# Kernel optimization log

Measured on AMD Instinct MI355X. Metric: run time of the kernel, lower is better.

Reference implementation:

```python
import jax, jax.numpy as jnp
import numpy as np

B, N, F, H, OUT = 64, 512, 128, 256, 6


def setup_inputs() -> dict:
    key = jax.random.key(0)
    ks = jax.random.split(key, 20)
    s = 0.02
    inp = {
        "x": jax.random.normal(ks[0], (B * N, F), dtype=jnp.float32),
        "edge_index": jax.random.randint(ks[1], (2, 16), 0, B * N),
        "edge_weight": jax.random.uniform(ks[2], (16,), dtype=jnp.float32),
        "batch": jnp.repeat(jnp.arange(B, dtype=jnp.int64), N),
        "sigma": jax.random.uniform(ks[3], (1,), dtype=jnp.float32),
        "Wg": s * jax.random.normal(ks[4], (F, F)), "bg": jnp.zeros((F,)),
        "Wrel0": s * jax.random.normal(ks[5], (F, H)), "Wroot0": s * jax.random.normal(ks[6], (F, H)), "brel0": jnp.zeros((H,)),
        "Wrel1": s * jax.random.normal(ks[7], (H, H)), "Wroot1": s * jax.random.normal(ks[8], (H, H)), "brel1": jnp.zeros((H,)),
        "Wrel2": s * jax.random.normal(ks[9], (H, H)), "Wroot2": s * jax.random.normal(ks[10], (H, H)), "brel2": jnp.zeros((H,)),
        "W1": s * jax.random.normal(ks[11], (H, H)), "b1": jnp.zeros((H,)),
        "Wout": s * jax.random.normal(ks[12], (H, OUT)), "bout": jnp.zeros((OUT,)),
    }
    return inp


def _forward(x, sigma, Wg, bg, Wrel0, Wroot0, brel0, Wrel1, Wroot1, brel1,
             Wrel2, Wroot2, brel2, W1, b1, Wout, bout):
    # gdmLinear
    h = x @ Wg + bg                      # [B*N, F]
    hw = h.reshape(B, N, -1)             # to_dense_batch (equal-size windows)
    # pairwise squared distances per window -> Gaussian kernel
    sq = jnp.sum(hw * hw, axis=-1)       # [B, N]
    dist = jnp.maximum(sq[:, :, None] + sq[:, None, :]
                       - 2.0 * jnp.einsum('bnf,bmf->bnm', hw, hw), 0.0)
    A = jnp.exp(-dist / (2.0 * sigma[0] ** 2))   # [B, N, N], all > 0
    A = A * (1.0 - jnp.eye(N, dtype=A.dtype))    # nonzero extraction drops self-loops

    def conv(h, Wrel, Wroot, brel):
        # GraphConv: out_i = W_rel @ sum_j A[j,i] * h_j + b_rel + W_root @ h_i
        agg = jnp.einsum('bji,bjf->bif', A, h)
        return agg @ Wrel + brel + h @ Wroot

    h = hw
    h = jax.nn.relu(conv(h, Wrel0, Wroot0, brel0))
    h = jax.nn.relu(conv(h, Wrel1, Wroot1, brel1))
    h = conv(h, Wrel2, Wroot2, brel2)
    g = jnp.mean(h, axis=1)              # global_mean_pool (equal-size graphs)
    g = jax.nn.relu(g @ W1 + b1)
    return g @ Wout + bout               # [B, OUT]


def reference(x, edge_index, edge_weight, batch, sigma, Wg, bg,
              Wrel0, Wroot0, brel0, Wrel1, Wroot1, brel1,
              Wrel2, Wroot2, brel2, W1, b1, Wout, bout):
    # edge_index / edge_weight / batch inputs are recomputed internally by GdmGNN
    return _forward(x, sigma, Wg, bg, Wrel0, Wroot0, brel0, Wrel1, Wroot1, brel1,
                    Wrel2, Wroot2, brel2, W1, b1, Wout, bout)
```

## Files before the change

### kernel.cpp

```cpp
#include <hip/hip_runtime.h>
#include <math.h>

#define Bsz 64
#define Nn 512
#define Ff 128
#define Hh 256
#define OUTD 6
#define MTOT (Bsz * Nn)

typedef __bf16 bf16x8 __attribute__((ext_vector_type(8)));
typedef float f32x4 __attribute__((ext_vector_type(4)));
typedef int int4v __attribute__((ext_vector_type(4)));
typedef unsigned short ushort4v __attribute__((ext_vector_type(4)));

__device__ __forceinline__ unsigned short f2bf(float f) {
    unsigned u = __float_as_uint(f);
    u += 0x7FFFu + ((u >> 16) & 1u);
    return (unsigned short)(u >> 16);
}
__device__ __forceinline__ float bf2f(unsigned short s) {
    return __uint_as_float(((unsigned)s) << 16);
}

#define SWZ(r) (((r) ^ ((r) >> 2)) & 3)

__device__ __forceinline__ void async_ld16(const unsigned short* g, unsigned short* l) {
    __builtin_amdgcn_global_load_lds(
        (const __attribute__((address_space(1))) void*)g,
        (__attribute__((address_space(3))) void*)l,
        16, 0, 0);
}

#define LDH 40
#define TSZ (128 * 32)
#define AGP 136
#define AGP1 264

__global__ __launch_bounds__(512) void fused_l0(
    const unsigned short* __restrict__ h0T,
    const unsigned short* __restrict__ Arows,
    const unsigned short* __restrict__ h0b,
    const unsigned short* __restrict__ WrelT0,
    const unsigned short* __restrict__ WrootT0,
    const float* __restrict__ brel0,
    unsigned short* __restrict__ h1b,
    unsigned short* __restrict__ h1T)
{
    int id = blockIdx.x;
    int b = id & 63;
    int nt = id >> 6;
    int n0g = nt * 128;
    long nodeBase = (long)b * Nn + n0g;

    const unsigned short* HT = h0T + (long)b * Ff * Nn;
    const unsigned short* AR = Arows + (long)b * Nn * Nn;

    __shared__ unsigned short SA[2 * TSZ];
    __shared__ unsigned short SB[2 * TSZ];
    __shared__ unsigned short aggL[128 * AGP];

    int tid = threadIdx.x;
    int lane = tid & 63;
    int wave = tid >> 6;
    int quad = lane >> 4, l16 = lane & 15;
    int wm = (wave >> 1) * 32, wn = (wave & 1) * 64;
    int sr = lane >> 2, sc = lane & 3;

    {
        f32x4 acc[2][4] = {};
        auto issue = [&](int g) {
            int kk = g << 5;
            unsigned short* Ad = SA + (g & 1) * TSZ;
            unsigned short* Bd = SB + (g & 1) * TSZ;
            int r = wave * 16 + sr;
            int c = sc ^ SWZ(r);
            async_ld16(HT + (long)r * Nn + kk + c * 8, Ad + (wave * 16) * 32);
            async_ld16(AR + (long)(n0g + r) * Nn + kk + c * 8, Bd + (wave * 16) * 32);
        };
        issue(0);
        for (int g = 0; g < (Nn >> 5); ++g) {
            __syncthreads();
            if (g + 1 < (Nn >> 5)) issue(g + 1);
            const unsigned short* Ab = SA + (g & 1) * TSZ;
            const unsigned short* Bb = SB + (g & 1) * TSZ;
            bf16x8 af[2], bfr[4];
            #pragma unroll
            for (int i = 0; i < 2; ++i) {
                int r = wm + i * 16 + l16;
                af[i] = *(const bf16x8*)&Ab[r * 32 + (quad ^ SWZ(r)) * 8];
            }
            #pragma unroll
            for (int j = 0; j < 4; ++j) {
                int r = wn + j * 16 + l16;
                bfr[j] = *(const bf16x8*)&Bb[r * 32 + (quad ^ SWZ(r)) * 8];
            }
            #pragma unroll
            for (int i = 0; i < 2; ++i)
                #pragma unroll
                for (int j = 0; j < 4; ++j)
                    acc[i][j] = __builtin_amdgcn_mfma_f32_16x16x32_bf16(
                        af[i], bfr[j], acc[i][j], 0, 0, 0);
        }
        #pragma unroll
        for (int i = 0; i < 2; ++i) {
            int f = wm + i * 16 + quad * 4;
            #pragma unroll
            for (int j = 0; j < 4; ++j) {
                int nl = wn + j * 16 + l16;
                f32x4 v = acc[i][j];
                ushort4v p;
                p[0] = f2bf(v[0]); p[1] = f2bf(v[1]);
                p[2] = f2bf(v[2]); p[3] = f2bf(v[3]);
                *(ushort4v*)&aggL[nl * AGP + f] = p;
            }
        }
    }
    __syncthreads();

    for (int half = 0; half < 2; ++half) {
        int m0 = half * 128;
        f32x4 acc[2][4] = {};
        auto issue = [&](int g) {
            unsigned short* Ad = SA + (g & 1) * TSZ;
            int r = wave * 16 + sr;
            int c = sc ^ SWZ(r);
            if (g < 4) {
                async_ld16(WrelT0 + (long)(m0 + r) * Ff + (g << 5) + c * 8,
                           Ad + (wave * 16) * 32);
            } else {
                async_ld16(WrootT0 + (long)(m0 + r) * Ff + ((g - 4) << 5) + c * 8,
                           Ad + (wave * 16) * 32);
                unsigned short* Bd = SB + (g & 1) * TSZ;
                async_ld16(h0b + (nodeBase + r) * Ff + ((g - 4) << 5) + c * 8,
                           Bd + (wave * 16) * 32);
            }
        };
        issue(0);
        for (int g = 0; g < 8; ++g) {
            __syncthreads();
            if (g + 1 < 8) issue(g + 1);
            const unsigned short* Ab = SA + (g & 1) * TSZ;
            bf16x8 af[2], bfr[4];
            #pragma unroll
            for (int i = 0; i < 2; ++i) {
                int r = wm + i * 16 + l16;
                af[i] = *(const bf16x8*)&Ab[r * 32 + (quad ^ SWZ(r)) * 8];
            }
            if (g < 4) {
                #pragma unroll
                for (int j = 0; j < 4; ++j) {
                    int nl = wn + j * 16 + l16;
                    bfr[j] = *(const bf16x8*)&aggL[nl * AGP + (g << 5) + quad * 8];
                }
            } else {
                const unsigned short* Bb = SB + (g & 1) * TSZ;
                #pragma unroll
                for (int j = 0; j < 4; ++j) {
                    int r = wn + j * 16 + l16;
                    bfr[j] = *(const bf16x8*)&Bb[r * 32 + (quad ^ SWZ(r)) * 8];
                }
            }
            #pragma unroll
            for (int i = 0; i < 2; ++i)
                #pragma unroll
                for (int j = 0; j < 4; ++j)
                    acc[i][j] = __builtin_amdgcn_mfma_f32_16x16x32_bf16(
                        af[i], bfr[j], acc[i][j], 0, 0, 0);
        }
        #pragma unroll
        for (int i = 0; i < 2; ++i) {
            int of = m0 + wm + i * 16 + quad * 4;
            float b0 = brel0[of + 0], b1 = brel0[of + 1];
            float b2 = brel0[of + 2], b3 = brel0[of + 3];
            #pragma unroll
            for (int j = 0; j < 4; ++j) {
                int nl = wn + j * 16 + l16;
                f32x4 v = acc[i][j];
                float o0 = fmaxf(v[0] + b0, 0.f), o1 = fmaxf(v[1] + b1, 0.f);
                float o2 = fmaxf(v[2] + b2, 0.f), o3 = fmaxf(v[3] + b3, 0.f);
                ushort4v p;
                p[0] = f2bf(o0); p[1] = f2bf(o1); p[2] = f2bf(o2); p[3] = f2bf(o3);
                *(ushort4v*)&h1b[(nodeBase + nl) * Hh + of] = p;
                long base = ((long)b * Hh) * 512 + n0g + nl;
                h1T[base + (long)(of + 0) * 512] = p[0];
                h1T[base + (long)(of + 1) * 512] = p[1];
                h1T[base + (long)(of + 2) * 512] = p[2];
                h1T[base + (long)(of + 3) * 512] = p[3];
            }
        }
    }
}

__global__ __launch_bounds__(512) void fused_l1(
    const unsigned short* __restrict__ h1T,
    const unsigned short* __restrict__ Arows,
    const unsigned short* __restrict__ h1b,
    const unsigned short* __restrict__ WrelT1,
    const unsigned short* __restrict__ WrootT1,
    const float* __restrict__ brel1,
    const float* __restrict__ w,
    float* __restrict__ vpart, float* __restrict__ mpart)
{
    constexpr int ATS = 256 * 32;
    constexpr int BTS = 64 * 32;

    int id = blockIdx.x;
    int b = id & 63;
    int nt = id >> 6;
    int n0g = nt * 64;
    long nodeBase = (long)b * Nn + n0g;

    const unsigned short* HT = h1T + (long)b * Hh * Nn;
    const unsigned short* AR = Arows + (long)b * Nn * Nn;

    __shared__ unsigned short SA[2 * ATS];
    __shared__ unsigned short SB[2 * BTS];
    __shared__ unsigned short aggL[64 * AGP1];

    int tid = threadIdx.x;
    int lane = tid & 63;
    int wave = tid >> 6;
    int quad = lane >> 4, l16 = lane & 15;
    int wm = wave * 32;
    int sr = lane >> 2, sc = lane & 3;

    {
        f32x4 acc[2][4] = {};
        auto issue = [&](int g) {
            int kk = g << 5;
            unsigned short* Ad = SA + (g & 1) * ATS;
            int r = wave * 16 + sr;
            int c = sc ^ SWZ(r);
            async_ld16(HT + (long)r * Nn + kk + c * 8, Ad + (wave * 16) * 32);
            int r2 = 128 + r;
            int c2 = sc ^ SWZ(r2);
            async_ld16(HT + (long)r2 * Nn + kk + c2 * 8, Ad + (128 + wave * 16) * 32);
            if (wave < 4) {
                unsigned short* Bd = SB + (g & 1) * BTS;
                async_ld16(AR + (long)(n0g + r) * Nn + kk + c * 8,
                           Bd + (wave * 16) * 32);
            }
        };
        issue(0);
        for (int g = 0; g < 16; ++g) {
            __syncthreads();
            if (g + 1 < 16) issue(g + 1);
            const unsigned short* Ab = SA + (g & 1) * ATS;
            const unsigned short* Bb = SB + (g & 1) * BTS;
            bf16x8 af[2], bfr[4];
            #pragma unroll
            for (int i = 0; i < 2; ++i) {
                int r = wm + i * 16 + l16;
                af[i] = *(const bf16x8*)&Ab[r * 32 + (quad ^ SWZ(r)) * 8];
            }
            #pragma unroll
            for (int j = 0; j < 4; ++j) {
                int r = j * 16 + l16;
                bfr[j] = *(const bf16x8*)&Bb[r * 32 + (quad ^ SWZ(r)) * 8];
            }
            #pragma unroll
            for (int i = 0; i < 2; ++i)
                #pragma unroll
                for (int j = 0; j < 4; ++j)
                    acc[i][j] = __builtin_amdgcn_mfma_f32_16x16x32_bf16(
                        af[i], bfr[j], acc[i][j], 0, 0, 0);
        }
        #pragma unroll
        for (int i = 0; i < 2; ++i) {
            int f = wm + i * 16 + quad * 4;
            #pragma unroll
            for (int j = 0; j < 4; ++j) {
                int nl = j * 16 + l16;
                f32x4 v = acc[i][j];
                ushort4v p;
                p[0] = f2bf(v[0]); p[1] = f2bf(v[1]);
                p[2] = f2bf(v[2]); p[3] = f2bf(v[3]);
                *(ushort4v*)&aggL[nl * AGP1 + f] = p;
            }
        }
    }
    __syncthreads();

    f32x4 acc[2][4] = {};
    auto issue2 = [&](int g) {
        const unsigned short* Wp = (g < 8) ? WrelT1 : WrootT1;
        int kk = (g & 7) << 5;
        unsigned short* Ad = SA + (g & 1) * ATS;
        int r = wave * 16 + sr;
        int c = sc ^ SWZ(r);
        async_ld16(Wp + (long)r * Hh + kk + c * 8, Ad + (wave * 16) * 32);
        int r2 = 128 + r;
        int c2 = sc ^ SWZ(r2);
        async_ld16(Wp + (long)r2 * Hh + kk + c2 * 8, Ad + (128 + wave * 16) * 32);
        if (g >= 8 && wave < 4) {
            unsigned short* Bd = SB + (g & 1) * BTS;
            async_ld16(h1b + (nodeBase + r) * Hh + kk + c * 8, Bd + (wave * 16) * 32);
        }
    };
    issue2(0);
    for (int g = 0; g < 16; ++g) {
        __syncthreads();
        if (g + 1 < 16) issue2(g + 1);
        const unsigned short* Ab = SA + (g & 1) * ATS;
        bf16x8 af[2], bfr[4];
        #pragma unroll
        for (int i = 0; i < 2; ++i) {
            int r = wm + i * 16 + l16;
            af[i] = *(const bf16x8*)&Ab[r * 32 + (quad ^ SWZ(r)) * 8];
        }
        if (g < 8) {
            #pragma unroll
            for (int j = 0; j < 4; ++j) {
                int nl = j * 16 + l16;
                bfr[j] = *(const bf16x8*)&aggL[nl * AGP1 + (g << 5) + quad * 8];
            }
        } else {
            const unsigned short* Bb = SB + (g & 1) * BTS;
            #pragma unroll
            for (int j = 0; j < 4; ++j) {
                int r = j * 16 + l16;
                bfr[j] = *(const bf16x8*)&Bb[r * 32 + (quad ^ SWZ(r)) * 8];
            }
        }
        #pragma unroll
        for (int i = 0; i < 2; ++i)
            #pragma unroll
            for (int j = 0; j < 4; ++j)
                acc[i][j] = __builtin_amdgcn_mfma_f32_16x16x32_bf16(
                    af[i], bfr[j], acc[i][j], 0, 0, 0);
    }

    #pragma unroll
    for (int i = 0; i < 2; ++i) {
        int lf = wm + i * 16 + quad * 4;
        float b0 = brel1[lf + 0], b1 = brel1[lf + 1];
        float b2 = brel1[lf + 2], b3 = brel1[lf + 3];
        float vp0 = 0.f, vp1 = 0.f, vp2 = 0.f, vp3 = 0.f;
        float mp0 = 0.f, mp1 = 0.f, mp2 = 0.f, mp3 = 0.f;
        #pragma unroll
        for (int j = 0; j < 4; ++j) {
            long node = nodeBase + j * 16 + l16;
            f32x4 v = acc[i][j];
            float o0 = fmaxf(v[0] + b0, 0.f), o1 = fmaxf(v[1] + b1, 0.f);
            float o2 = fmaxf(v[2] + b2, 0.f), o3 = fmaxf(v[3] + b3, 0.f);
            float h0v = bf2f(f2bf(o0)), h1v = bf2f(f2bf(o1));
            float h2v = bf2f(f2bf(o2)), h3v = bf2f(f2bf(o3));
            float wv = w[node];
            vp0 += wv * h0v; vp1 += wv * h1v; vp2 += wv * h2v; vp3 += wv * h3v;
            mp0 += h0v; mp1 += h1v; mp2 += h2v; mp3 += h3v;
        }
        #pragma unroll
        for (int m = 1; m < 16; m <<= 1) {
            vp0 += __shfl_xor(vp0, m); vp1 += __shfl_xor(vp1, m);
            vp2 += __shfl_xor(vp2, m); vp3 += __shfl_xor(vp3, m);
            mp0 += __shfl_xor(mp0, m); mp1 += __shfl_xor(mp1, m);
            mp2 += __shfl_xor(mp2, m); mp3 += __shfl_xor(mp3, m);
        }
        if (l16 == 0) {
            long o = ((long)(b * 8 + nt)) * Hh + lf;
            float4 vv = {vp0, vp1, vp2, vp3};
            float4 mm = {mp0, mp1, mp2, mp3};
            *(float4*)&vpart[o] = vv;
            *(float4*)&mpart[o] = mm;
        }
    }
}

__global__ __launch_bounds__(256) void prep_h0(
    const float* __restrict__ x, const float* __restrict__ Wg,
    const float* __restrict__ bg,
    const float* __restrict__ Wrel0, const float* __restrict__ Wroot0,
    const float* __restrict__ Wrel1, const float* __restrict__ Wroot1,
    unsigned short* __restrict__ T0, unsigned short* __restrict__ T1,
    unsigned short* __restrict__ T2, unsigned short* __restrict__ T3,
    float* __restrict__ w,
    unsigned short* __restrict__ h0b, unsigned short* __restrict__ h0T,
    float* __restrict__ sqv)
{
    if (blockIdx.x < 896) {
        int idx = blockIdx.x * 256 + threadIdx.x;
        if (idx >= 196608) { w[idx - 196608] = 0.f; return; }
        const float* src; unsigned short* dst; int kin; int e;
        if      (idx <  32768) { src = Wrel0;  dst = T0; kin = 128; e = idx; }
        else if (idx <  65536) { src = Wroot0; dst = T1; kin = 128; e = idx - 32768; }
        else if (idx < 131072) { src = Wrel1;  dst = T2; kin = 256; e = idx - 65536; }
        else                   { src = Wroot1; dst = T3; kin = 256; e = idx - 131072; }
        int o = (kin == 128) ? (e >> 7) : (e >> 8);
        int i = e & (kin - 1);
        dst[e] = f2bf(src[(long)i * 256 + o]);
        return;
    }

    __shared__ unsigned short As[128 * LDH];
    __shared__ unsigned short Bs[128 * LDH];
    __shared__ float rsq[128];

    int tid = threadIdx.x;
    int lane = tid & 63;
    int wave = tid >> 6;
    int quad = lane >> 4, l16 = lane & 15;
    int wm = (wave >> 1) * 64, wn = (wave & 1) * 64;
    int m0 = (blockIdx.x - 896) * 128;

    f32x4 acc[4][4] = {};

    for (int k0 = 0; k0 < Ff; k0 += 32) {
        __syncthreads();
        #pragma unroll
        for (int l = 0; l < 2; ++l) {
            int idx = tid + l * 256;
            int r = idx >> 2, ch = idx & 3;
            const float* px = x + (long)(m0 + r) * Ff + k0 + ch * 8;
            float4 xa = *(const float4*)px;
            float4 xb = *(const float4*)(px + 4);
            ushort4v pa, pb;
            pa[0] = f2bf(xa.x); pa[1] = f2bf(xa.y); pa[2] = f2bf(xa.z); pa[3] = f2bf(xa.w);
            pb[0] = f2bf(xb.x); pb[1] = f2bf(xb.y); pb[2] = f2bf(xb.z); pb[3] = f2bf(xb.w);
            *(ushort4v*)&As[r * LDH + ch * 8] = pa;
            *(ushort4v*)&As[r * LDH + ch * 8 + 4] = pb;
            int kk = k0 + ch * 8;
            ushort4v qa, qb;
            #pragma unroll
            for (int u = 0; u < 4; ++u) qa[u] = f2bf(Wg[(long)(kk + u) * 128 + r]);
            #pragma unroll
            for (int u = 0; u < 4; ++u) qb[u] = f2bf(Wg[(long)(kk + 4 + u) * 128 + r]);
            *(ushort4v*)&Bs[r * LDH + ch * 8] = qa;
            *(ushort4v*)&Bs[r * LDH + ch * 8 + 4] = qb;
        }
        __syncthreads();
        bf16x8 af[4], bfr[4];
        #pragma unroll
        for (int i = 0; i < 4; ++i)
            af[i] = *(const bf16x8*)&As[(wm + i * 16 + l16) * LDH + quad * 8];
        #pragma unroll
        for (int j = 0; j < 4; ++j)
            bfr[j] = *(const bf16x8*)&Bs[(wn + j * 16 + l16) * LDH + quad * 8];
        #pragma unroll
        for (int i = 0; i < 4; ++i)
            #pragma unroll
            for (int j = 0; j < 4; ++j)
                acc[i][j] = __builtin_amdgcn_mfma_f32_16x16x32_bf16(
                    af[i], bfr[j], acc[i][j], 0, 0, 0);
    }

    if (tid < 128) rsq[tid] = 0.f;
    __syncthreads();

    #pragma unroll
    for (int i = 0; i < 4; ++i) {
        int lrow = wm + i * 16 + quad * 4;
        int mb = m0 + lrow;
        float rp0 = 0.f, rp1 = 0.f, rp2 = 0.f, rp3 = 0.f;
        #pragma unroll
        for (int j = 0; j < 4; ++j) {
            int n = wn + j * 16 + l16;
            f32x4 v = acc[i][j];
            float bv = bg[n];
            unsigned short s0 = f2bf(v[0] + bv), s1 = f2bf(v[1] + bv);
            unsigned short s2 = f2bf(v[2] + bv), s3 = f2bf(v[3] + bv);
            h0b[(long)(mb + 0) * Ff + n] = s0;
            h0b[(long)(mb + 1) * Ff + n] = s1;
            h0b[(long)(mb + 2) * Ff + n] = s2;
            h0b[(long)(mb + 3) * Ff + n] = s3;
            ushort4v p; p[0] = s0; p[1] = s1; p[2] = s2; p[3] = s3;
            long ti = ((long)(mb >> 9) * Ff + n) * 512 + (mb & 511);
            *(ushort4v*)&h0T[ti] = p;
            float f0 = bf2f(s0), f1 = bf2f(s1), f2 = bf2f(s2), f3 = bf2f(s3);
            rp0 += f0 * f0; rp1 += f1 * f1; rp2 += f2 * f2; rp3 += f3 * f3;
        }
        #pragma unroll
        for (int m = 1; m < 16; m <<= 1) {
            rp0 += __shfl_xor(rp0, m);
            rp1 += __shfl_xor(rp1, m);
            rp2 += __shfl_xor(rp2, m);
            rp3 += __shfl_xor(rp3, m);
        }
        if (l16 == 0) {
            atomicAdd(&rsq[lrow + 0], rp0);
            atomicAdd(&rsq[lrow + 1], rp1);
            atomicAdd(&rsq[lrow + 2], rp2);
            atomicAdd(&rsq[lrow + 3], rp3);
        }
    }
    __syncthreads();
    if (tid < 128) sqv[m0 + tid] = rsq[tid];
}

__global__ __launch_bounds__(512) void gram_A_mfma(
    const unsigned short* __restrict__ h0b, const float* __restrict__ sqv,
    const float* __restrict__ sigma, unsigned short* __restrict__ Aout,
    float* __restrict__ w)
{
    int id = blockIdx.x;
    int b = id & 63;
    int t = id >> 6;
    int i0 = (t & 3) * 128, j0 = (t >> 2) * 128;

    const unsigned short* H = h0b + (long)b * Nn * Ff;
    const float* SQ = sqv + (long)b * Nn;
    unsigned short* Ab = Aout + (long)b * Nn * Nn;

    __shared__ unsigned short Is[2 * TSZ];
    __shared__ unsigned short Js[2 * TSZ];
    __shared__ float rsum[128];

    int tid = threadIdx.x;
    int lane = tid & 63;
    int wave = tid >> 6;
    int quad = lane >> 4, l16 = lane & 15;
    int wm = (wave >> 1) * 32, wn = (wave & 1) * 64;

    int sr = lane >> 2, sc = lane & 3;

    f32x4 acc[2][4] = {};

    auto issue = [&](int g) {
        int kk = g << 5;
        unsigned short* Id = Is + (g & 1) * TSZ;
        unsigned short* Jd = Js + (g & 1) * TSZ;
        int r = wave * 16 + sr;
        int c = sc ^ SWZ(r);
        async_ld16(H + (long)(i0 + r) * Ff + kk + c * 8, Id + (wave * 16) * 32);
        async_ld16(H + (long)(j0 + r) * Ff + kk + c * 8, Jd + (wave * 16) * 32);
    };

    issue(0);
    for (int g = 0; g < (Ff >> 5); ++g) {
        __syncthreads();
        if (g + 1 < (Ff >> 5)) issue(g + 1);
        const unsigned short* Ib = Is + (g & 1) * TSZ;
        const unsigned short* Jb = Js + (g & 1) * TSZ;
        bf16x8 af[2], bfr[4];
        #pragma unroll
        for (int i = 0; i < 2; ++i) {
            int r = wm + i * 16 + l16;
            af[i] = *(const bf16x8*)&Ib[r * 32 + (quad ^ SWZ(r)) * 8];
        }
        #pragma unroll
        for (int j = 0; j < 4; ++j) {
            int r = wn + j * 16 + l16;
            bfr[j] = *(const bf16x8*)&Jb[r * 32 + (quad ^ SWZ(r)) * 8];
        }
        #pragma unroll
        for (int i = 0; i < 2; ++i)
            #pragma unroll
            for (int j = 0; j < 4; ++j)
                acc[i][j] = __builtin_amdgcn_mfma_f32_16x16x32_bf16(
                    af[i], bfr[j], acc[i][j], 0, 0, 0);
    }

    if (tid < 128) rsum[tid] = 0.f;
    __syncthreads();

    float s = sigma[0];
    float inv2s2 = 1.0f / (2.0f * s * s);
    #pragma unroll
    for (int i = 0; i < 2; ++i) {
        int lrow = wm + i * 16 + quad * 4;
        int rb = i0 + lrow;
        float rs0 = 0.f, rs1 = 0.f, rs2 = 0.f, rs3 = 0.f;
        #pragma unroll
        for (int j = 0; j < 4; ++j) {
            int c = j0 + wn + j * 16 + l16;
            float sqc = SQ[c];
            f32x4 v = acc[i][j];
            ushort4v pk;
            float av[4];
            #pragma unroll
            for (int r4 = 0; r4 < 4; ++r4) {
                int r = rb + r4;
                float d = fmaxf(SQ[r] + sqc - 2.0f * v[r4], 0.0f);
                unsigned short a = (r == c) ? (unsigned short)0
                                            : f2bf(__expf(-d * inv2s2));
                pk[r4] = a;
                av[r4] = bf2f(a);
            }
            *(ushort4v*)&Ab[(long)c * Nn + rb] = pk;
            rs0 += av[0]; rs1 += av[1]; rs2 += av[2]; rs3 += av[3];
        }
        #pragma unroll
        for (int m = 1; m < 16; m <<= 1) {
            rs0 += __shfl_xor(rs0, m);
            rs1 += __shfl_xor(rs1, m);
            rs2 += __shfl_xor(rs2, m);
            rs3 += __shfl_xor(rs3, m);
        }
        if (l16 == 0) {
            atomicAdd(&rsum[lrow + 0], rs0);
            atomicAdd(&rsum[lrow + 1], rs1);
            atomicAdd(&rsum[lrow + 2], rs2);
            atomicAdd(&rsum[lrow + 3], rs3);
        }
    }
    __syncthreads();
    if (tid < 128) atomicAdd(&w[(long)b * Nn + i0 + tid], rsum[tid]);
}

__global__ __launch_bounds__(256) void head_kernel(
    const float* __restrict__ vpart, const float* __restrict__ mpart,
    const float* __restrict__ Wrel2, const float* __restrict__ Wroot2,
    const float* __restrict__ brel2,
    const float* __restrict__ W1, const float* __restrict__ b1,
    const float* __restrict__ Wout, const float* __restrict__ bout,
    float* __restrict__ out)
{
    int b = blockIdx.x;
    int j = threadIdx.x;
    __shared__ float vs[Hh], ms[Hh], gs[Hh], g2[Hh];
    float vp = 0.f, mp = 0.f;
    #pragma unroll
    for (int p = 0; p < 8; ++p) {
        long o = ((long)(b * 8 + p)) * Hh + j;
        vp += vpart[o];
        mp += mpart[o];
    }
    vs[j] = vp * (1.0f / (float)Nn);
    ms[j] = mp * (1.0f / (float)Nn);
    __syncthreads();
    float s = brel2[j];
    for (int c = 0; c < Hh; ++c)
        s += vs[c] * Wrel2[c * Hh + j] + ms[c] * Wroot2[c * Hh + j];
    gs[j] = s;
    __syncthreads();
    float t = b1[j];
    for (int k = 0; k < Hh; ++k) t += gs[k] * W1[k * Hh + j];
    g2[j] = fmaxf(t, 0.f);
    __syncthreads();
    if (j < OUTD) {
        float s2 = bout[j];
        for (int k = 0; k < Hh; ++k) s2 += g2[k] * Wout[k * OUTD + j];
        out[b * OUTD + j] = s2;
    }
}

extern "C" void kernel_launch(void* const* d_in, const int* in_sizes, int n_in,
                              void* d_out, int out_size, void* d_ws, size_t ws_size,
                              hipStream_t stream) {
    const float* x      = (const float*)d_in[0];
    const float* sigma  = (const float*)d_in[4];
    const float* Wg     = (const float*)d_in[5];
    const float* bg     = (const float*)d_in[6];
    const float* Wrel0  = (const float*)d_in[7];
    const float* Wroot0 = (const float*)d_in[8];
    const float* brel0  = (const float*)d_in[9];
    const float* Wrel1  = (const float*)d_in[10];
    const float* Wroot1 = (const float*)d_in[11];
    const float* brel1  = (const float*)d_in[12];
    const float* Wrel2  = (const float*)d_in[13];
    const float* Wroot2 = (const float*)d_in[14];
    const float* brel2  = (const float*)d_in[15];
    const float* W1     = (const float*)d_in[16];
    const float* b1     = (const float*)d_in[17];
    const float* Wout   = (const float*)d_in[18];
    const float* bout   = (const float*)d_in[19];
    float* out = (float*)d_out;

    char* ws = (char*)d_ws;
    unsigned short* h0b  = (unsigned short*)(ws + 16777216);
    unsigned short* h0T  = (unsigned short*)(ws + 25165824);
    float*          sq   = (float*)(ws + 33554432);
    unsigned short* Aadj = (unsigned short*)(ws + 33685504);
    unsigned short* h1b  = (unsigned short*)(ws + 84017152);
    unsigned short* h1T  = (unsigned short*)(ws + 100794368);
    unsigned short* WrelT0  = (unsigned short*)(ws + 167903232);
    unsigned short* WrootT0 = (unsigned short*)(ws + 167968768);
    unsigned short* WrelT1  = (unsigned short*)(ws + 168034304);
    unsigned short* WrootT1 = (unsigned short*)(ws + 168165376);
    float*          w     = (float*)(ws + 168558592);
    float*          vpart = (float*)(ws + 168689664);
    float*          mpart = (float*)(ws + 169213952);

    prep_h0<<<1152, 256, 0, stream>>>(x, Wg, bg, Wrel0, Wroot0, Wrel1, Wroot1,
                                      WrelT0, WrootT0, WrelT1, WrootT1,
                                      w, h0b, h0T, sq);

    gram_A_mfma<<<dim3(16 * Bsz, 1, 1), 512, 0, stream>>>(h0b, sq, sigma, Aadj, w);

    fused_l0<<<dim3(4 * Bsz, 1, 1), 512, 0, stream>>>(
        h0T, Aadj, h0b, WrelT0, WrootT0, brel0, h1b, h1T);

    fused_l1<<<dim3(8 * Bsz, 1, 1), 512, 0, stream>>>(
        h1T, Aadj, h1b, WrelT1, WrootT1, brel1, w, vpart, mpart);

    head_kernel<<<Bsz, 256, 0, stream>>>(vpart, mpart, Wrel2, Wroot2, brel2,
                                         W1, b1, Wout, bout, out);
}
```

Measured before the change: 210.6 us.

## Enlarge per-block tiles in fused GraphConv layers to compute all outputs at once

fused_l0's second phase now computes all 256 output features in one pass using a 4x4 MFMA accumulator per wave, instead of two 128-feature halves that each reloaded the root input tile. fused_l1 doubles its node tile from 64 to 128 per block, halving the grid to 256 blocks so each weight and h1T tile is reused across more nodes. Partial pooling sums are written per wave-half to keep the vpart/mpart layout. The cost is more accumulator registers, more LDS per block (larger aggL and buffers) and fewer blocks, which lowers occupancy and parallelism.

```diff
diff --git a/kernel.cpp b/kernel.cpp
--- a/kernel.cpp
+++ b/kernel.cpp
@@ -33,6 +33,7 @@
 
 #define LDH 40
 #define TSZ (128 * 32)
+#define ATS (256 * 32)
 #define AGP 136
 #define AGP1 264
 
@@ -55,7 +56,7 @@
     const unsigned short* HT = h0T + (long)b * Ff * Nn;
     const unsigned short* AR = Arows + (long)b * Nn * Nn;
 
-    __shared__ unsigned short SA[2 * TSZ];
+    __shared__ unsigned short SA[2 * ATS];
     __shared__ unsigned short SB[2 * TSZ];
     __shared__ unsigned short aggL[128 * AGP];
 
@@ -63,14 +64,14 @@
     int lane = tid & 63;
     int wave = tid >> 6;
     int quad = lane >> 4, l16 = lane & 15;
-    int wm = (wave >> 1) * 32, wn = (wave & 1) * 64;
     int sr = lane >> 2, sc = lane & 3;
 
     {
+        int wm = (wave >> 1) * 32, wn = (wave & 1) * 64;
         f32x4 acc[2][4] = {};
         auto issue = [&](int g) {
             int kk = g << 5;
-            unsigned short* Ad = SA + (g & 1) * TSZ;
+            unsigned short* Ad = SA + (g & 1) * ATS;
             unsigned short* Bd = SB + (g & 1) * TSZ;
             int r = wave * 16 + sr;
             int c = sc ^ SWZ(r);
@@ -81,7 +82,7 @@
         for (int g = 0; g < (Nn >> 5); ++g) {
             __syncthreads();
             if (g + 1 < (Nn >> 5)) issue(g + 1);
-            const unsigned short* Ab = SA + (g & 1) * TSZ;
+            const unsigned short* Ab = SA + (g & 1) * ATS;
             const unsigned short* Bb = SB + (g & 1) * TSZ;
             bf16x8 af[2], bfr[4];
             #pragma unroll
@@ -117,32 +118,33 @@
     }
     __syncthreads();
 
-    for (int half = 0; half < 2; ++half) {
-        int m0 = half * 128;
-        f32x4 acc[2][4] = {};
-        auto issue = [&](int g) {
-            unsigned short* Ad = SA + (g & 1) * TSZ;
+    {
+        int wm = (wave >> 1) * 64, wn = (wave & 1) * 64;
+        f32x4 acc[4][4] = {};
+        auto issue2 = [&](int g) {
+            const unsigned short* Wp = (g < 4) ? WrelT0 : WrootT0;
+            int kk = (g & 3) << 5;
+            unsigned short* Ad = SA + (g & 1) * ATS;
             int r = wave * 16 + sr;
             int c = sc ^ SWZ(r);
-            if (g < 4) {
-                async_ld16(WrelT0 + (long)(m0 + r) * Ff + (g << 5) + c * 8,
-                           Ad + (wave * 16) * 32);
-            } else {
-                async_ld16(WrootT0 + (long)(m0 + r) * Ff + ((g - 4) << 5) + c * 8,
-                           Ad + (wave * 16) * 32);
+            async_ld16(Wp + (long)r * Ff + kk + c * 8, Ad + (wave * 16) * 32);
+            int r2 = 128 + r;
+            int c2 = sc ^ SWZ(r2);
+            async_ld16(Wp + (long)r2 * Ff + kk + c2 * 8, Ad + (128 + wave * 16) * 32);
+            if (g >= 4) {
                 unsigned short* Bd = SB + (g & 1) * TSZ;
-                async_ld16(h0b + (nodeBase + r) * Ff + ((g - 4) << 5) + c * 8,
+                async_ld16(h0b + (nodeBase + r) * Ff + kk + c * 8,
                            Bd + (wave * 16) * 32);
             }
         };
-        issue(0);
+        issue2(0);
         for (int g = 0; g < 8; ++g) {
             __syncthreads();
-            if (g + 1 < 8) issue(g + 1);
-            const unsigned short* Ab = SA + (g & 1) * TSZ;
-            bf16x8 af[2], bfr[4];
-            #pragma unroll
-            for (int i = 0; i < 2; ++i) {
+            if (g + 1 < 8) issue2(g + 1);
+            const unsigned short* Ab = SA + (g & 1) * ATS;
+            bf16x8 af[4], bfr[4];
+            #pragma unroll
+            for (int i = 0; i < 4; ++i) {
                 int r = wm + i * 16 + l16;
                 af[i] = *(const bf16x8*)&Ab[r * 32 + (quad ^ SWZ(r)) * 8];
             }
@@ -161,15 +163,15 @@
                 }
             }
             #pragma unroll
-            for (int i = 0; i < 2; ++i)
+            for (int i = 0; i < 4; ++i)
                 #pragma unroll
                 for (int j = 0; j < 4; ++j)
                     acc[i][j] = __builtin_amdgcn_mfma_f32_16x16x32_bf16(
                         af[i], bfr[j], acc[i][j], 0, 0, 0);
         }
         #pragma unroll
-        for (int i = 0; i < 2; ++i) {
-            int of = m0 + wm + i * 16 + quad * 4;
+        for (int i = 0; i < 4; ++i) {
+            int of = wm + i * 16 + quad * 4;
             float b0 = brel0[of + 0], b1 = brel0[of + 1];
             float b2 = brel0[of + 2], b3 = brel0[of + 3];
             #pragma unroll
@@ -201,13 +203,12 @@
     const float* __restrict__ w,
     float* __restrict__ vpart, float* __restrict__ mpart)
 {
-    constexpr int ATS = 256 * 32;
-    constexpr int BTS = 64 * 32;
+    constexpr int BTS = 128 * 32;
 
     int id = blockIdx.x;
     int b = id & 63;
     int nt = id >> 6;
-    int n0g = nt * 64;
+    int n0g = nt * 128;
     long nodeBase = (long)b * Nn + n0g;
 
     const unsigned short* HT = h1T + (long)b * Hh * Nn;
@@ -215,17 +216,18 @@
 
     __shared__ unsigned short SA[2 * ATS];
     __shared__ unsigned short SB[2 * BTS];
-    __shared__ unsigned short aggL[64 * AGP1];
+    __shared__ unsigned short aggL[128 * AGP1];
 
     int tid = threadIdx.x;
     int lane = tid & 63;
     int wave = tid >> 6;
     int quad = lane >> 4, l16 = lane & 15;
-    int wm = wave * 32;
+    int wm = (wave >> 1) * 64;
+    int wn = (wave & 1) * 64;
     int sr = lane >> 2, sc = lane & 3;
 
     {
-        f32x4 acc[2][4] = {};
+        f32x4 acc[4][4] = {};
         auto issue = [&](int g) {
             int kk = g << 5;
             unsigned short* Ad = SA + (g & 1) * ATS;
@@ -235,11 +237,8 @@
             int r2 = 128 + r;
             int c2 = sc ^ SWZ(r2);
             async_ld16(HT + (long)r2 * Nn + kk + c2 * 8, Ad + (128 + wave * 16) * 32);
-            if (wave < 4) {
-                unsigned short* Bd = SB + (g & 1) * BTS;
-                async_ld16(AR + (long)(n0g + r) * Nn + kk + c * 8,
-                           Bd + (wave * 16) * 32);
-            }
+            unsigned short* Bd = SB + (g & 1) * BTS;
+            async_ld16(AR + (long)(n0g + r) * Nn + kk + c * 8, Bd + (wave * 16) * 32);
         };
         issue(0);
         for (int g = 0; g < 16; ++g) {
@@ -247,30 +246,30 @@
             if (g + 1 < 16) issue(g + 1);
             const unsigned short* Ab = SA + (g & 1) * ATS;
             const unsigned short* Bb = SB + (g & 1) * BTS;
-            bf16x8 af[2], bfr[4];
-            #pragma unroll
-            for (int i = 0; i < 2; ++i) {
+            bf16x8 af[4], bfr[4];
+            #pragma unroll
+            for (int i = 0; i < 4; ++i) {
                 int r = wm + i * 16 + l16;
                 af[i] = *(const bf16x8*)&Ab[r * 32 + (quad ^ SWZ(r)) * 8];
             }
             #pragma unroll
             for (int j = 0; j < 4; ++j) {
-                int r = j * 16 + l16;
+                int r = wn + j * 16 + l16;
                 bfr[j] = *(const bf16x8*)&Bb[r * 32 + (quad ^ SWZ(r)) * 8];
             }
             #pragma unroll
-            for (int i = 0; i < 2; ++i)
+            for (int i = 0; i < 4; ++i)
                 #pragma unroll
                 for (int j = 0; j < 4; ++j)
                     acc[i][j] = __builtin_amdgcn_mfma_f32_16x16x32_bf16(
                         af[i], bfr[j], acc[i][j], 0, 0, 0);
         }
         #pragma unroll
-        for (int i = 0; i < 2; ++i) {
+        for (int i = 0; i < 4; ++i) {
             int f = wm + i * 16 + quad * 4;
             #pragma unroll
             for (int j = 0; j < 4; ++j) {
-                int nl = j * 16 + l16;
+                int nl = wn + j * 16 + l16;
                 f32x4 v = acc[i][j];
                 ushort4v p;
                 p[0] = f2bf(v[0]); p[1] = f2bf(v[1]);
@@ -281,7 +280,7 @@
     }
     __syncthreads();
 
-    f32x4 acc[2][4] = {};
+    f32x4 acc[4][4] = {};
     auto issue2 = [&](int g) {
         const unsigned short* Wp = (g < 8) ? WrelT1 : WrootT1;
         int kk = (g & 7) << 5;
@@ -292,7 +291,7 @@
         int r2 = 128 + r;
         int c2 = sc ^ SWZ(r2);
         async_ld16(Wp + (long)r2 * Hh + kk + c2 * 8, Ad + (128 + wave * 16) * 32);
-        if (g >= 8 && wave < 4) {
+        if (g >= 8) {
             unsigned short* Bd = SB + (g & 1) * BTS;
             async_ld16(h1b + (nodeBase + r) * Hh + kk + c * 8, Bd + (wave * 16) * 32);
         }
@@ -302,28 +301,28 @@
         __syncthreads();
         if (g + 1 < 16) issue2(g + 1);
         const unsigned short* Ab = SA + (g & 1) * ATS;
-        bf16x8 af[2], bfr[4];
-        #pragma unroll
-        for (int i = 0; i < 2; ++i) {
+        bf16x8 af[4], bfr[4];
+        #pragma unroll
+        for (int i = 0; i < 4; ++i) {
             int r = wm + i * 16 + l16;
             af[i] = *(const bf16x8*)&Ab[r * 32 + (quad ^ SWZ(r)) * 8];
         }
         if (g < 8) {
             #pragma unroll
             for (int j = 0; j < 4; ++j) {
-                int nl = j * 16 + l16;
+                int nl = wn + j * 16 + l16;
                 bfr[j] = *(const bf16x8*)&aggL[nl * AGP1 + (g << 5) + quad * 8];
             }
         } else {
             const unsigned short* Bb = SB + (g & 1) * BTS;
             #pragma unroll
             for (int j = 0; j < 4; ++j) {
-                int r = j * 16 + l16;
+                int r = wn + j * 16 + l16;
                 bfr[j] = *(const bf16x8*)&Bb[r * 32 + (quad ^ SWZ(r)) * 8];
             }
         }
         #pragma unroll
-        for (int i = 0; i < 2; ++i)
+        for (int i = 0; i < 4; ++i)
             #pragma unroll
             for (int j = 0; j < 4; ++j)
                 acc[i][j] = __builtin_amdgcn_mfma_f32_16x16x32_bf16(
@@ -331,7 +330,7 @@
     }
 
     #pragma unroll
-    for (int i = 0; i < 2; ++i) {
+    for (int i = 0; i < 4; ++i) {
         int lf = wm + i * 16 + quad * 4;
         float b0 = brel1[lf + 0], b1 = brel1[lf + 1];
         float b2 = brel1[lf + 2], b3 = brel1[lf + 3];
@@ -339,7 +338,7 @@
         float mp0 = 0.f, mp1 = 0.f, mp2 = 0.f, mp3 = 0.f;
         #pragma unroll
         for (int j = 0; j < 4; ++j) {
-            long node = nodeBase + j * 16 + l16;
+            long node = nodeBase + wn + j * 16 + l16;
             f32x4 v = acc[i][j];
             float o0 = fmaxf(v[0] + b0, 0.f), o1 = fmaxf(v[1] + b1, 0.f);
             float o2 = fmaxf(v[2] + b2, 0.f), o3 = fmaxf(v[3] + b3, 0.f);
@@ -357,7 +356,7 @@
             mp2 += __shfl_xor(mp2, m); mp3 += __shfl_xor(mp3, m);
         }
         if (l16 == 0) {
-            long o = ((long)(b * 8 + nt)) * Hh + lf;
+            long o = ((long)(b * 8 + nt * 2 + (wave & 1))) * Hh + lf;
             float4 vv = {vp0, vp1, vp2, vp3};
             float4 mm = {mp0, mp1, mp2, mp3};
             *(float4*)&vpart[o] = vv;
@@ -679,7 +678,7 @@
     fused_l0<<<dim3(4 * Bsz, 1, 1), 512, 0, stream>>>(
         h0T, Aadj, h0b, WrelT0, WrootT0, brel0, h1b, h1T);
 
-    fused_l1<<<dim3(8 * Bsz, 1, 1), 512, 0, stream>>>(
+    fused_l1<<<dim3(4 * Bsz, 1, 1), 512, 0, stream>>>(
         h1T, Aadj, h1b, WrelT1, WrootT1, brel1, w, vpart, mpart);
 
     head_kernel<<<Bsz, 256, 0, stream>>>(vpart, mpart, Wrel2, Wroot2, brel2,
```

Result: no change. 211.5 us (+0.4%).
